# Kernel tuning notes

Measured on AMD Instinct MI355X. Metric: run time of the kernel, lower is better.

The kernel has to match this reference:

```python
import jax, jax.numpy as jnp
import numpy as np

C = 1.0            # PoincareBall curvature
BALL_EPS = 4e-3    # geoopt projx eps for float32
MIN_NORM = 1e-15


def artanh(x):
    x = jnp.clip(x, -1.0 + 1e-7, 1.0 - 1e-7)
    return 0.5 * (jnp.log1p(x) - jnp.log1p(-x))


def project(x):
    # geoopt projx: clip norm to (1 - eps) / sqrt(c)
    norm = jnp.maximum(jnp.linalg.norm(x, axis=-1, keepdims=True), MIN_NORM)
    maxnorm = (1.0 - BALL_EPS) / jnp.sqrt(C)
    return jnp.where(norm > maxnorm, x / norm * maxnorm, x)


def mobius_matvec(M, x):
    # geoopt mobius_matvec on PoincareBall (followed by project)
    sqrt_c = jnp.sqrt(C)
    x_norm = jnp.maximum(jnp.linalg.norm(x, axis=-1, keepdims=True), MIN_NORM)
    mx = x @ M.T
    mx_norm = jnp.maximum(jnp.linalg.norm(mx, axis=-1, keepdims=True), MIN_NORM)
    res = jnp.tanh(mx_norm / x_norm * artanh(sqrt_c * x_norm)) * mx / (mx_norm * sqrt_c)
    zero_mx = jnp.all(mx == 0.0, axis=-1, keepdims=True)
    return project(jnp.where(zero_mx, 0.0, res))


def mobius_add(x, y):
    # geoopt mobius_add on PoincareBall (followed by project)
    x2 = jnp.sum(x * x, axis=-1, keepdims=True)
    y2 = jnp.sum(y * y, axis=-1, keepdims=True)
    xy = jnp.sum(x * y, axis=-1, keepdims=True)
    num = (1.0 + 2.0 * C * xy + C * y2) * x + (1.0 - C * x2) * y
    den = jnp.maximum(1.0 + 2.0 * C * xy + C * C * x2 * y2, MIN_NORM)
    return project(num / den)


def hyp_linear(x, W, b):
    out = mobius_matvec(W, x)
    return mobius_add(out, b)


def hyperbolic_scores(q, k):
    # q, k: [B, H, S, Dh]
    eps = 1e-5
    q_norm_sq = jnp.minimum(jnp.sum(q * q, axis=-1, keepdims=True), 1.0 - eps)  # [B,H,S,1]
    k_norm_sq = jnp.minimum(jnp.sum(k * k, axis=-1, keepdims=True), 1.0 - eps)  # [B,H,S,1]
    qk = jnp.einsum('bhqd,bhkd->bhqk', q, k)
    k_norm_sq_t = jnp.swapaxes(k_norm_sq, -2, -1)                               # [B,H,1,S]
    denom = (1.0 - q_norm_sq) * (1.0 - k_norm_sq_t) + eps
    delta = 2.0 * ((qk - q_norm_sq * k_norm_sq_t) / denom)
    dist_sq = jnp.sqrt(jnp.maximum(delta, eps))
    return -dist_sq


def setup_inputs() -> dict:
    key = jax.random.key(0)
    B, S, E = 4, 2048, 512
    ks = jax.random.split(key, 5)
    x = jax.random.normal(ks[0], (B, S, E), dtype=jnp.float32) * 0.02  # inside unit ball
    bound = float(np.sqrt(6.0 / (E + E)))  # xavier_uniform
    def w(k):
        return jax.random.uniform(k, (E, E), dtype=jnp.float32, minval=-bound, maxval=bound)
    z = jnp.zeros((E,), dtype=jnp.float32)
    return {
        'x': x,
        'Wq': w(ks[1]), 'bq': z,
        'Wk': w(ks[2]), 'bk': z,
        'Wv': w(ks[3]), 'bv': z,
        'Wo': w(ks[4]), 'bo': z,
    }


def reference(x, Wq, bq, Wk, bk, Wv, bv, Wo, bo):
    B, S, E = x.shape
    H = 8
    Dh = E // H
    q = hyp_linear(x, Wq, bq)
    k = hyp_linear(x, Wk, bk)
    v = hyp_linear(x, Wv, bv)
    # [B,S,E] -> [B,H,S,Dh]
    split = lambda t: t.reshape(B, S, H, Dh).transpose(0, 2, 1, 3)
    q, k, v = split(q), split(k), split(v)
    scores = hyperbolic_scores(q, k) / jnp.sqrt(jnp.float32(Dh))
    attn = jax.nn.softmax(scores, axis=-1)
    out = jnp.einsum('bhqk,bhkd->bhqd', attn, v)
    out = out.transpose(0, 2, 1, 3).reshape(B, S, E)
    return hyp_linear(out, Wo, bo)
```

## Files before the change

kernel.cpp:

```cpp
#include <hip/hip_runtime.h>
#include <math.h>

#define B_ 4
#define S_ 2048
#define E_ 512
#define H_ 8
#define Dh_ 64
#define BS_ (B_*S_)
#define MAXN 0.996f

typedef __attribute__((ext_vector_type(8))) short short8;
typedef __attribute__((ext_vector_type(4))) float f32x4;

__device__ __forceinline__ unsigned f2bf(float x) {
  unsigned u = __float_as_uint(x);
  return (u + 0x7fffu + ((u >> 16) & 1u)) >> 16;
}
__device__ __forceinline__ float bf2f(unsigned b) {
  return __uint_as_float(b << 16);
}

__device__ __forceinline__ void gload_lds16(const void* g, void* lds) {
  __builtin_amdgcn_global_load_lds(
      (const __attribute__((address_space(1))) unsigned int*)g,
      (__attribute__((address_space(3))) unsigned int*)lds, 16, 0, 0);
}

__global__ __launch_bounds__(256) void pack_w_kernel(const float* __restrict__ W0,
    const float* __restrict__ W1, const float* __restrict__ W2,
    const float* __restrict__ W3, unsigned short* __restrict__ Wp) {
  const float* W = (blockIdx.y == 0) ? W0 : (blockIdx.y == 1) ? W1
                 : (blockIdx.y == 2) ? W2 : W3;
  unsigned short* dst = Wp + (size_t)blockIdx.y * 262144;
  int l = threadIdx.x & 63, tq = threadIdx.x >> 6;
  int n = blockIdx.x;
  int col = 16*n + (l & 15);
  int k0 = 8 * (l >> 4);
  #pragma unroll
  for (int tt = 0; tt < 4; ++tt) {
    int t = tq*4 + tt;
    const float* wp_ = W + (size_t)col * E_ + 32*t + k0;
    float4 a0 = *(const float4*)wp_, a1 = *(const float4*)(wp_ + 4);
    float av[8] = {a0.x,a0.y,a0.z,a0.w,a1.x,a1.y,a1.z,a1.w};
    short8 hi;
    #pragma unroll
    for (int j = 0; j < 8; ++j) hi[j] = (short)f2bf(av[j]);
    *(short8*)(dst + ((size_t)(t*32 + n))*512 + l*8) = hi;
  }
}

__global__ __launch_bounds__(256, 4) void qkv_linear(const float* __restrict__ X,
    const unsigned short* __restrict__ Wp,
    const float* __restrict__ bq_, const float* __restrict__ bk_,
    const float* __restrict__ bv_,
    unsigned short* __restrict__ Qhi, unsigned short* __restrict__ Khi,
    unsigned short* __restrict__ Vhi,
    float* __restrict__ qn, float* __restrict__ kn) {
  __shared__ float smM[4][4][4], smB[4][4][4], smb2[4];
  int tid = threadIdx.x;
  int w = tid >> 6, l = tid & 63;
  int l15 = l & 15, g = l >> 4;
  int R = blockIdx.x;
  int mat = blockIdx.y;
  const unsigned short* Wm = Wp + (size_t)mat * 262144;
  const float* bvec = (mat == 0) ? bq_ : (mat == 1) ? bk_ : bv_;
  unsigned short* outHi = (mat == 0) ? Qhi : (mat == 1) ? Khi : Vhi;
  float* normOut = (mat == 0) ? qn : kn;

  f32x4 acc[8];
  #pragma unroll
  for (int s = 0; s < 8; ++s) acc[s] = (f32x4){0.f,0.f,0.f,0.f};
  const float* xrow = X + (size_t)(R*16 + l15)*E_ + 8*g;

  float4 c0 = *(const float4*)xrow;
  float4 c1 = *(const float4*)(xrow + 4);
  float xsq = 0.f;

  #pragma unroll 2
  for (int t = 0; t < 16; ++t) {
    float av[8] = {c0.x,c0.y,c0.z,c0.w,c1.x,c1.y,c1.z,c1.w};
    short8 ahi, alo;
    #pragma unroll
    for (int j = 0; j < 8; ++j) {
      unsigned hb = f2bf(av[j]);
      ahi[j] = (short)hb;
      alo[j] = (short)f2bf(av[j] - bf2f(hb));
      xsq = fmaf(av[j], av[j], xsq);
    }
    if (t < 15) {
      c0 = *(const float4*)(xrow + 32*(t+1));
      c1 = *(const float4*)(xrow + 32*(t+1) + 4);
    }
    const unsigned short* wb = Wm + ((size_t)(t*32 + 8*w))*512 + (size_t)l*8;
    #pragma unroll
    for (int s = 0; s < 8; ++s) {
      short8 bhi = *(const short8*)(wb + s*512);
      acc[s] = __builtin_amdgcn_mfma_f32_16x16x32_bf16(ahi, bhi, acc[s], 0, 0, 0);
      acc[s] = __builtin_amdgcn_mfma_f32_16x16x32_bf16(alo, bhi, acc[s], 0, 0, 0);
    }
  }

  xsq += __shfl_xor(xsq, 16, 64);
  xsq += __shfl_xor(xsq, 32, 64);
  float xnv4[4], art4[4];
  #pragma unroll
  for (int i = 0; i < 4; ++i) {
    float s2 = __shfl(xsq, 4*g + i, 64);
    float xnv = fmaxf(sqrtf(s2), 1e-15f);
    float aa = fminf(xnv, 1.f - 1e-7f);
    xnv4[i] = xnv;
    art4[i] = 0.5f * (log1pf(aa) - log1pf(-aa));
  }

  float bl[8];
  #pragma unroll
  for (int s = 0; s < 8; ++s) bl[s] = bvec[16*(8*w+s) + l15];
  float m2p[4] = {0.f,0.f,0.f,0.f}, mbp[4] = {0.f,0.f,0.f,0.f}, b2p = 0.f;
  #pragma unroll
  for (int s = 0; s < 8; ++s) {
    b2p += bl[s]*bl[s];
    #pragma unroll
    for (int i = 0; i < 4; ++i) {
      m2p[i] = fmaf(acc[s][i], acc[s][i], m2p[i]);
      mbp[i] = fmaf(acc[s][i], bl[s], mbp[i]);
    }
  }
  #pragma unroll
  for (int off = 1; off <= 8; off <<= 1) {
    b2p += __shfl_xor(b2p, off, 64);
    #pragma unroll
    for (int i = 0; i < 4; ++i) {
      m2p[i] += __shfl_xor(m2p[i], off, 64);
      mbp[i] += __shfl_xor(mbp[i], off, 64);
    }
  }
  if (l == 0) smb2[w] = b2p;
  if (l15 == 0) {
    #pragma unroll
    for (int i = 0; i < 4; ++i) { smM[w][g][i] = m2p[i]; smB[w][g][i] = mbp[i]; }
  }
  __syncthreads();
  float b2 = smb2[0] + smb2[1] + smb2[2] + smb2[3];
  float G[4], Hc[4];
  #pragma unroll
  for (int i = 0; i < 4; ++i) {
    float m2 = smM[0][g][i]+smM[1][g][i]+smM[2][g][i]+smM[3][g][i];
    float mb = smB[0][g][i]+smB[1][g][i]+smB[2][g][i]+smB[3][g][i];
    float xn = xnv4[i], art = art4[i];
    float mn = fmaxf(sqrtf(m2), 1e-15f);
    float t = tanhf(mn / xn * art);
    float alpha, rn;
    if (m2 > 0.f) { alpha = t / mn; rn = t; } else { alpha = 0.f; rn = 0.f; }
    if (rn > MAXN) { alpha *= MAXN / rn; rn = MAXN; }
    float x2r = rn * rn;
    float xy = alpha * mb;
    float A  = 1.f + 2.f*xy + b2;
    float Bc = 1.f - x2r;
    float den = fmaxf(1.f + 2.f*xy + x2r*b2, 1e-15f);
    float n2v = (A*A*x2r + 2.f*A*Bc*xy + Bc*Bc*b2) / (den*den);
    float nn = fmaxf(sqrtf(n2v), 1e-15f);
    float sc = (nn > MAXN) ? (MAXN / nn) : 1.f;
    G[i]  = sc * A * alpha / den;
    Hc[i] = sc * Bc / den;
  }

  #pragma unroll
  for (int i = 0; i < 4; ++i) {
    int grow = R*16 + 4*g + i;
    int bb = grow >> 11, seq = grow & 2047;
    int tile = seq >> 6;
    float hn0 = 0.f, hn1 = 0.f;
    #pragma unroll
    for (int s = 0; s < 8; ++s) {
      int col = 16*(8*w+s) + l15;
      float v = G[i]*acc[s][i] + Hc[i]*bl[s];
      int h = col >> 6, c = col & 63;
      size_t base;
      if (mat == 2) {
        int kt = (seq >> 5) & 1, gp = (seq >> 3) & 3, jv = seq & 7;
        int dn = c >> 4, lt = (c & 15) | (gp << 4);
        base = ((size_t)((bb*8 + h)*32 + tile))*4096 + (size_t)((kt*4+dn)*64 + lt)*8 + jv;
      } else {
        int nf = (seq >> 4) & 3, lt15 = seq & 15;
        int dt = c >> 5, m = (c >> 3) & 3, j = c & 7;
        base = ((size_t)((bb*8 + h)*32 + tile))*4096 + (size_t)((dt*4+nf)*64 + (lt15|(m<<4)))*8 + j;
      }
      outHi[base] = (unsigned short)f2bf(v);
      if (mat < 2) { if (s < 4) hn0 += v*v; else hn1 += v*v; }
    }
    if (mat < 2) {
      hn0 += __shfl_xor(hn0,1,64); hn0 += __shfl_xor(hn0,2,64);
      hn0 += __shfl_xor(hn0,4,64); hn0 += __shfl_xor(hn0,8,64);
      hn1 += __shfl_xor(hn1,1,64); hn1 += __shfl_xor(hn1,2,64);
      hn1 += __shfl_xor(hn1,4,64); hn1 += __shfl_xor(hn1,8,64);
      if (l15 == 0) {
        normOut[((size_t)(bb*8 + 2*w + 0))*S_ + seq] = fminf(hn0, 1.f - 1e-5f);
        normOut[((size_t)(bb*8 + 2*w + 1))*S_ + seq] = fminf(hn1, 1.f - 1e-5f);
      }
    }
  }
}

__global__ __launch_bounds__(256, 4) void o_linear(const float* __restrict__ X,
    const unsigned short* __restrict__ Wp, const float* __restrict__ bvec,
    float* __restrict__ outF) {
  __shared__ float smM[4][4][4], smB[4][4][4], smb2[4];
  int tid = threadIdx.x;
  int w = tid >> 6, l = tid & 63;
  int l15 = l & 15, g = l >> 4;
  int R = blockIdx.x;

  f32x4 acc[8];
  #pragma unroll
  for (int s = 0; s < 8; ++s) acc[s] = (f32x4){0.f,0.f,0.f,0.f};
  const float* xrow = X + (size_t)(R*16 + l15)*E_ + 8*g;

  float4 c0 = *(const float4*)xrow;
  float4 c1 = *(const float4*)(xrow + 4);
  float xsq = 0.f;

  #pragma unroll 2
  for (int t = 0; t < 16; ++t) {
    float av[8] = {c0.x,c0.y,c0.z,c0.w,c1.x,c1.y,c1.z,c1.w};
    short8 ahi, alo;
    #pragma unroll
    for (int j = 0; j < 8; ++j) {
      unsigned hb = f2bf(av[j]);
      ahi[j] = (short)hb;
      alo[j] = (short)f2bf(av[j] - bf2f(hb));
      xsq = fmaf(av[j], av[j], xsq);
    }
    if (t < 15) {
      c0 = *(const float4*)(xrow + 32*(t+1));
      c1 = *(const float4*)(xrow + 32*(t+1) + 4);
    }
    const unsigned short* wb = Wp + ((size_t)(t*32 + 8*w))*512 + (size_t)l*8;
    #pragma unroll
    for (int s = 0; s < 8; ++s) {
      short8 bhi = *(const short8*)(wb + s*512);
      acc[s] = __builtin_amdgcn_mfma_f32_16x16x32_bf16(ahi, bhi, acc[s], 0, 0, 0);
      acc[s] = __builtin_amdgcn_mfma_f32_16x16x32_bf16(alo, bhi, acc[s], 0, 0, 0);
    }
  }

  xsq += __shfl_xor(xsq, 16, 64);
  xsq += __shfl_xor(xsq, 32, 64);
  float xnv4[4], art4[4];
  #pragma unroll
  for (int i = 0; i < 4; ++i) {
    float s2 = __shfl(xsq, 4*g + i, 64);
    float xnv = fmaxf(sqrtf(s2), 1e-15f);
    float aa = fminf(xnv, 1.f - 1e-7f);
    xnv4[i] = xnv;
    art4[i] = 0.5f * (log1pf(aa) - log1pf(-aa));
  }

  float bl[8];
  #pragma unroll
  for (int s = 0; s < 8; ++s) bl[s] = bvec[16*(8*w+s) + l15];
  float m2p[4] = {0.f,0.f,0.f,0.f}, mbp[4] = {0.f,0.f,0.f,0.f}, b2p = 0.f;
  #pragma unroll
  for (int s = 0; s < 8; ++s) {
    b2p += bl[s]*bl[s];
    #pragma unroll
    for (int i = 0; i < 4; ++i) {
      m2p[i] = fmaf(acc[s][i], acc[s][i], m2p[i]);
      mbp[i] = fmaf(acc[s][i], bl[s], mbp[i]);
    }
  }
  #pragma unroll
  for (int off = 1; off <= 8; off <<= 1) {
    b2p += __shfl_xor(b2p, off, 64);
    #pragma unroll
    for (int i = 0; i < 4; ++i) {
      m2p[i] += __shfl_xor(m2p[i], off, 64);
      mbp[i] += __shfl_xor(mbp[i], off, 64);
    }
  }
  if (l == 0) smb2[w] = b2p;
  if (l15 == 0) {
    #pragma unroll
    for (int i = 0; i < 4; ++i) { smM[w][g][i] = m2p[i]; smB[w][g][i] = mbp[i]; }
  }
  __syncthreads();
  float b2 = smb2[0] + smb2[1] + smb2[2] + smb2[3];
  #pragma unroll
  for (int i = 0; i < 4; ++i) {
    float m2 = smM[0][g][i]+smM[1][g][i]+smM[2][g][i]+smM[3][g][i];
    float mb = smB[0][g][i]+smB[1][g][i]+smB[2][g][i]+smB[3][g][i];
    float xn = xnv4[i], art = art4[i];
    float mn = fmaxf(sqrtf(m2), 1e-15f);
    float t = tanhf(mn / xn * art);
    float alpha, rn;
    if (m2 > 0.f) { alpha = t / mn; rn = t; } else { alpha = 0.f; rn = 0.f; }
    if (rn > MAXN) { alpha *= MAXN / rn; rn = MAXN; }
    float x2r = rn * rn;
    float xy = alpha * mb;
    float A  = 1.f + 2.f*xy + b2;
    float Bc = 1.f - x2r;
    float den = fmaxf(1.f + 2.f*xy + x2r*b2, 1e-15f);
    float n2v = (A*A*x2r + 2.f*A*Bc*xy + Bc*Bc*b2) / (den*den);
    float nn = fmaxf(sqrtf(n2v), 1e-15f);
    float sc = (nn > MAXN) ? (MAXN / nn) : 1.f;
    float G = sc * A * alpha / den;
    float Hc = sc * Bc / den;
    int grow = R*16 + 4*g + i;
    #pragma unroll
    for (int s = 0; s < 8; ++s)
      outF[(size_t)grow*E_ + 16*(8*w+s) + l15] = G*acc[s][i] + Hc*bl[s];
  }
}

__global__ __launch_bounds__(256, 4) void attn_kernel(
    const unsigned short* __restrict__ Qhi, const unsigned short* __restrict__ Khi,
    const unsigned short* __restrict__ Vhi,
    const float* __restrict__ qn_arr, const float* __restrict__ kn_arr,
    float* __restrict__ Out) {
  __shared__ __align__(16) unsigned short Kf[4096];
  __shared__ __align__(16) unsigned short Vf[2][4096];
  __shared__ __align__(16) unsigned short Pf[4][1024];

  int tid = threadIdx.x;
  int w = tid >> 6, l = tid & 63;
  int l15 = l & 15, g = l >> 4;

  int bid = blockIdx.x;
  int xcd = bid & 7, idx = bid >> 3;
  int bh = xcd * 4 + (idx >> 5);
  int qblk = idx & 31;
  int b = bh >> 3, h = bh & 7;
  int qb = qblk * 64;

  const unsigned short* qbase = Qhi + ((size_t)(bh*32 + qblk))*4096;
  short8 qhi[2];
  #pragma unroll
  for (int dt = 0; dt < 2; ++dt)
    qhi[dt] = *(const short8*)(qbase + (size_t)((dt*4 + w)*64 + l)*8);
  float qnv[4], qd[4], rq[4];
  #pragma unroll
  for (int i = 0; i < 4; ++i) {
    qnv[i] = qn_arr[(size_t)bh*S_ + qb + 16*w + 4*g + i];
    qd[i] = 1.f - qnv[i];
    rq[i] = __builtin_amdgcn_rcpf(qd[i]);
  }

  f32x4 Oacc[4];
  #pragma unroll
  for (int dn = 0; dn < 4; ++dn) Oacc[dn] = (f32x4){0.f,0.f,0.f,0.f};
  float lp[4] = {0.f,0.f,0.f,0.f};

  const unsigned short* Kbh = Khi + ((size_t)bh*32)*4096;
  const unsigned short* Vbh = Vhi + ((size_t)bh*32)*4096;
  const float* knp = kn_arr + (size_t)bh*S_;

  #pragma unroll
  for (int r = 0; r < 2; ++r) {
    gload_lds16(Kbh + r*2048 + w*512 + l*8, &Kf[r*2048 + w*512]);
    gload_lds16(Vbh + r*2048 + w*512 + l*8, &Vf[0][r*2048 + w*512]);
  }
  asm volatile("s_waitcnt vmcnt(0)" ::: "memory");
  __syncthreads();

  #pragma unroll 1
  for (int tile = 0; tile < 32; ++tile) {
    int cur = tile & 1;
    int kb = tile * 64;
    float knc[4];
    #pragma unroll
    for (int n = 0; n < 4; ++n) knc[n] = knp[kb + 16*n + l15];
    #pragma unroll
    for (int n = 0; n < 4; ++n) {
      f32x4 Cn = (f32x4){0.f,0.f,0.f,0.f};
      #pragma unroll
      for (int dt = 0; dt < 2; ++dt) {
        short8 kfr = *(const short8*)&Kf[((dt*4 + n)*64 + l)*8];
        Cn = __builtin_amdgcn_mfma_f32_16x16x32_bf16(qhi[dt], kfr, Cn, 0, 0, 0);
      }
      float kd = 1.f - knc[n];
      float rkn = __builtin_amdgcn_rcpf(kd);
      int cbase = (n >> 1)*64 + 16*((2*n + (l15 >> 3)) & 3) + 4*g;
      int csb = cbase ^ ((cbase >> 3) & 7);
      int j7 = l15 & 7;
      #pragma unroll
      for (int i = 0; i < 4; ++i) {
        float num = fmaf(-qnv[i], knc[n], Cn[i]);
        float d2 = fmaxf(num * (rq[i]*rkn), 5e-6f);
        float sq = d2 * __builtin_amdgcn_rsqf(d2);
        float p = __builtin_amdgcn_exp2f(-0.25503386f * sq);
        unsigned u = __float_as_uint(p);
        lp[i] += __uint_as_float(u & 0xffff0000u);
        Pf[w][((csb ^ i) << 3) + j7] = (unsigned short)(u >> 16);
      }
    }
    __builtin_amdgcn_s_barrier();
    if (tile < 31) {
      const unsigned short* kp = Kbh + ((size_t)(tile+1))*4096;
      const unsigned short* vp = Vbh + ((size_t)(tile+1))*4096;
      #pragma unroll
      for (int r = 0; r < 2; ++r)
        gload_lds16(kp + r*2048 + w*512 + l*8, &Kf[r*2048 + w*512]);
      #pragma unroll
      for (int r = 0; r < 2; ++r)
        gload_lds16(vp + r*2048 + w*512 + l*8, &Vf[cur^1][r*2048 + w*512]);
    }
    __builtin_amdgcn_sched_barrier(0);
    short8 pa0, pa1;
    { int c = l;       int cs = c ^ ((c >> 3) & 7); pa0 = *(const short8*)&Pf[w][cs*8]; }
    { int c = 64 + l;  int cs = c ^ ((c >> 3) & 7); pa1 = *(const short8*)&Pf[w][cs*8]; }
    #pragma unroll
    for (int dn = 0; dn < 4; ++dn) {
      short8 v0 = *(const short8*)&Vf[cur][((0*4 + dn)*64 + l)*8];
      short8 v1 = *(const short8*)&Vf[cur][((1*4 + dn)*64 + l)*8];
      f32x4 o = Oacc[dn];
      o = __builtin_amdgcn_mfma_f32_16x16x32_bf16(pa0, v0, o, 0, 0, 0);
      o = __builtin_amdgcn_mfma_f32_16x16x32_bf16(pa1, v1, o, 0, 0, 0);
      Oacc[dn] = o;
    }
    asm volatile("s_waitcnt vmcnt(2)" ::: "memory");
    __builtin_amdgcn_s_barrier();
  }

  #pragma unroll
  for (int i = 0; i < 4; ++i) {
    lp[i] += __shfl_xor(lp[i], 1, 64);
    lp[i] += __shfl_xor(lp[i], 2, 64);
    lp[i] += __shfl_xor(lp[i], 4, 64);
    lp[i] += __shfl_xor(lp[i], 8, 64);
    lp[i] = 1.f / lp[i];
  }
  #pragma unroll
  for (int i = 0; i < 4; ++i) {
    size_t orow = (size_t)(b*S_ + qb + 16*w + 4*g + i)*E_ + h*Dh_;
    #pragma unroll
    for (int dn = 0; dn < 4; ++dn)
      Out[orow + 16*dn + l15] = Oacc[dn][i] * lp[i];
  }
}

extern "C" void kernel_launch(void* const* d_in, const int* in_sizes, int n_in,
                              void* d_out, int out_size, void* d_ws, size_t ws_size,
                              hipStream_t stream) {
  const float* x  = (const float*)d_in[0];
  const float* Wq = (const float*)d_in[1];
  const float* bq = (const float*)d_in[2];
  const float* Wk = (const float*)d_in[3];
  const float* bk = (const float*)d_in[4];
  const float* Wv = (const float*)d_in[5];
  const float* bv = (const float*)d_in[6];
  const float* Wo = (const float*)d_in[7];
  const float* bo = (const float*)d_in[8];
  float* out = (float*)d_out;

  char* p = (char*)d_ws;
  unsigned short* Wp  = (unsigned short*)p; p += (size_t)2  << 20;
  unsigned short* Qhi = (unsigned short*)p; p += (size_t)8  << 20;
  unsigned short* Khi = (unsigned short*)p; p += (size_t)8  << 20;
  unsigned short* Vhi = (unsigned short*)p; p += (size_t)8  << 20;
  float* ao   = (float*)p; p += (size_t)16 << 20;
  float* qn   = (float*)p; p += (size_t)B_*H_*S_ * 4;
  float* kn   = (float*)p; p += (size_t)B_*H_*S_ * 4;

  pack_w_kernel<<<dim3(32, 4), dim3(256), 0, stream>>>(Wq, Wk, Wv, Wo, Wp);
  qkv_linear<<<dim3(BS_/16, 3), dim3(256), 0, stream>>>(x, Wp, bq, bk, bv, Qhi, Khi, Vhi, qn, kn);
  attn_kernel<<<dim3(1024), dim3(256), 0, stream>>>(Qhi, Khi, Vhi, qn, kn, ao);
  o_linear<<<dim3(BS_/16), dim3(256), 0, stream>>>(ao, Wp + 3*262144, bo, out);
}
```

Before: 167.8 us.

## Process 32 rows per block in linear kernels to reuse weight fragments

The QKV and output linear kernels now compute two 16-row tiles per block, so each weight fragment loaded from global memory feeds twice as many MFMAs. This halves the grid size and the total weight traffic. The loop is no longer unrolled and all weight fragments are loaded up front. Register pressure rises from doubling the accumulators, so launch bounds drop from 4 to 3 blocks per CU, which lowers occupancy and the number of blocks available to hide latency.

```diff
diff --git a/kernel.cpp b/kernel.cpp
--- a/kernel.cpp
+++ b/kernel.cpp
@@ -49,14 +49,14 @@
   }
 }
 
-__global__ __launch_bounds__(256, 4) void qkv_linear(const float* __restrict__ X,
+__global__ __launch_bounds__(256, 3) void qkv_linear(const float* __restrict__ X,
     const unsigned short* __restrict__ Wp,
     const float* __restrict__ bq_, const float* __restrict__ bk_,
     const float* __restrict__ bv_,
     unsigned short* __restrict__ Qhi, unsigned short* __restrict__ Khi,
     unsigned short* __restrict__ Vhi,
     float* __restrict__ qn, float* __restrict__ kn) {
-  __shared__ float smM[4][4][4], smB[4][4][4], smb2[4];
+  __shared__ float smM[2][4][4][4], smB[2][4][4][4], smb2[4];
   int tid = threadIdx.x;
   int w = tid >> 6, l = tid & 63;
   int l15 = l & 15, g = l >> 4;
@@ -67,247 +67,311 @@
   unsigned short* outHi = (mat == 0) ? Qhi : (mat == 1) ? Khi : Vhi;
   float* normOut = (mat == 0) ? qn : kn;
 
-  f32x4 acc[8];
-  #pragma unroll
-  for (int s = 0; s < 8; ++s) acc[s] = (f32x4){0.f,0.f,0.f,0.f};
-  const float* xrow = X + (size_t)(R*16 + l15)*E_ + 8*g;
-
-  float4 c0 = *(const float4*)xrow;
-  float4 c1 = *(const float4*)(xrow + 4);
-  float xsq = 0.f;
-
-  #pragma unroll 2
+  f32x4 acc0[8], acc1[8];
+  #pragma unroll
+  for (int s = 0; s < 8; ++s) {
+    acc0[s] = (f32x4){0.f,0.f,0.f,0.f};
+    acc1[s] = (f32x4){0.f,0.f,0.f,0.f};
+  }
+  const float* xrow0 = X + (size_t)(R*32 + l15)*E_ + 8*g;
+  const float* xrow1 = xrow0 + (size_t)16*E_;
+  const unsigned short* wl = Wm + (size_t)(8*w)*512 + (size_t)l*8;
+
+  float4 p00 = *(const float4*)xrow0, p01 = *(const float4*)(xrow0 + 4);
+  float4 p10 = *(const float4*)xrow1, p11 = *(const float4*)(xrow1 + 4);
+  float xsq0 = 0.f, xsq1 = 0.f;
+
+  #pragma unroll 1
   for (int t = 0; t < 16; ++t) {
-    float av[8] = {c0.x,c0.y,c0.z,c0.w,c1.x,c1.y,c1.z,c1.w};
-    short8 ahi, alo;
+    const unsigned short* wb = wl + (size_t)t*16384;
+    short8 b[8];
+    #pragma unroll
+    for (int s = 0; s < 8; ++s) b[s] = *(const short8*)(wb + s*512);
+    float a0v[8] = {p00.x,p00.y,p00.z,p00.w,p01.x,p01.y,p01.z,p01.w};
+    float a1v[8] = {p10.x,p10.y,p10.z,p10.w,p11.x,p11.y,p11.z,p11.w};
+    short8 ahi0, alo0, ahi1, alo1;
     #pragma unroll
     for (int j = 0; j < 8; ++j) {
-      unsigned hb = f2bf(av[j]);
-      ahi[j] = (short)hb;
-      alo[j] = (short)f2bf(av[j] - bf2f(hb));
-      xsq = fmaf(av[j], av[j], xsq);
+      unsigned hb0 = f2bf(a0v[j]);
+      ahi0[j] = (short)hb0;
+      alo0[j] = (short)f2bf(a0v[j] - bf2f(hb0));
+      xsq0 = fmaf(a0v[j], a0v[j], xsq0);
+      unsigned hb1 = f2bf(a1v[j]);
+      ahi1[j] = (short)hb1;
+      alo1[j] = (short)f2bf(a1v[j] - bf2f(hb1));
+      xsq1 = fmaf(a1v[j], a1v[j], xsq1);
     }
     if (t < 15) {
-      c0 = *(const float4*)(xrow + 32*(t+1));
-      c1 = *(const float4*)(xrow + 32*(t+1) + 4);
-    }
-    const unsigned short* wb = Wm + ((size_t)(t*32 + 8*w))*512 + (size_t)l*8;
+      p00 = *(const float4*)(xrow0 + 32*(t+1));
+      p01 = *(const float4*)(xrow0 + 32*(t+1) + 4);
+      p10 = *(const float4*)(xrow1 + 32*(t+1));
+      p11 = *(const float4*)(xrow1 + 32*(t+1) + 4);
+    }
     #pragma unroll
     for (int s = 0; s < 8; ++s) {
-      short8 bhi = *(const short8*)(wb + s*512);
-      acc[s] = __builtin_amdgcn_mfma_f32_16x16x32_bf16(ahi, bhi, acc[s], 0, 0, 0);
-      acc[s] = __builtin_amdgcn_mfma_f32_16x16x32_bf16(alo, bhi, acc[s], 0, 0, 0);
-    }
-  }
-
-  xsq += __shfl_xor(xsq, 16, 64);
-  xsq += __shfl_xor(xsq, 32, 64);
-  float xnv4[4], art4[4];
+      acc0[s] = __builtin_amdgcn_mfma_f32_16x16x32_bf16(ahi0, b[s], acc0[s], 0, 0, 0);
+      acc0[s] = __builtin_amdgcn_mfma_f32_16x16x32_bf16(alo0, b[s], acc0[s], 0, 0, 0);
+      acc1[s] = __builtin_amdgcn_mfma_f32_16x16x32_bf16(ahi1, b[s], acc1[s], 0, 0, 0);
+      acc1[s] = __builtin_amdgcn_mfma_f32_16x16x32_bf16(alo1, b[s], acc1[s], 0, 0, 0);
+    }
+  }
+
+  xsq0 += __shfl_xor(xsq0, 16, 64); xsq0 += __shfl_xor(xsq0, 32, 64);
+  xsq1 += __shfl_xor(xsq1, 16, 64); xsq1 += __shfl_xor(xsq1, 32, 64);
+  float xnv4[2][4], art4[2][4];
   #pragma unroll
   for (int i = 0; i < 4; ++i) {
-    float s2 = __shfl(xsq, 4*g + i, 64);
-    float xnv = fmaxf(sqrtf(s2), 1e-15f);
-    float aa = fminf(xnv, 1.f - 1e-7f);
-    xnv4[i] = xnv;
-    art4[i] = 0.5f * (log1pf(aa) - log1pf(-aa));
+    float s20 = __shfl(xsq0, 4*g + i, 64);
+    float s21 = __shfl(xsq1, 4*g + i, 64);
+    float xn0 = fmaxf(sqrtf(s20), 1e-15f);
+    float xn1 = fmaxf(sqrtf(s21), 1e-15f);
+    float aa0 = fminf(xn0, 1.f - 1e-7f);
+    float aa1 = fminf(xn1, 1.f - 1e-7f);
+    xnv4[0][i] = xn0; art4[0][i] = 0.5f * (log1pf(aa0) - log1pf(-aa0));
+    xnv4[1][i] = xn1; art4[1][i] = 0.5f * (log1pf(aa1) - log1pf(-aa1));
   }
 
   float bl[8];
   #pragma unroll
   for (int s = 0; s < 8; ++s) bl[s] = bvec[16*(8*w+s) + l15];
-  float m2p[4] = {0.f,0.f,0.f,0.f}, mbp[4] = {0.f,0.f,0.f,0.f}, b2p = 0.f;
+  float m2p[2][4] = {{0.f,0.f,0.f,0.f},{0.f,0.f,0.f,0.f}};
+  float mbp[2][4] = {{0.f,0.f,0.f,0.f},{0.f,0.f,0.f,0.f}};
+  float b2p = 0.f;
   #pragma unroll
   for (int s = 0; s < 8; ++s) {
     b2p += bl[s]*bl[s];
     #pragma unroll
     for (int i = 0; i < 4; ++i) {
-      m2p[i] = fmaf(acc[s][i], acc[s][i], m2p[i]);
-      mbp[i] = fmaf(acc[s][i], bl[s], mbp[i]);
+      m2p[0][i] = fmaf(acc0[s][i], acc0[s][i], m2p[0][i]);
+      mbp[0][i] = fmaf(acc0[s][i], bl[s], mbp[0][i]);
+      m2p[1][i] = fmaf(acc1[s][i], acc1[s][i], m2p[1][i]);
+      mbp[1][i] = fmaf(acc1[s][i], bl[s], mbp[1][i]);
     }
   }
   #pragma unroll
   for (int off = 1; off <= 8; off <<= 1) {
     b2p += __shfl_xor(b2p, off, 64);
     #pragma unroll
-    for (int i = 0; i < 4; ++i) {
-      m2p[i] += __shfl_xor(m2p[i], off, 64);
-      mbp[i] += __shfl_xor(mbp[i], off, 64);
-    }
+    for (int rg = 0; rg < 2; ++rg)
+      #pragma unroll
+      for (int i = 0; i < 4; ++i) {
+        m2p[rg][i] += __shfl_xor(m2p[rg][i], off, 64);
+        mbp[rg][i] += __shfl_xor(mbp[rg][i], off, 64);
+      }
   }
   if (l == 0) smb2[w] = b2p;
   if (l15 == 0) {
     #pragma unroll
-    for (int i = 0; i < 4; ++i) { smM[w][g][i] = m2p[i]; smB[w][g][i] = mbp[i]; }
+    for (int rg = 0; rg < 2; ++rg)
+      #pragma unroll
+      for (int i = 0; i < 4; ++i) { smM[rg][w][g][i] = m2p[rg][i]; smB[rg][w][g][i] = mbp[rg][i]; }
   }
   __syncthreads();
   float b2 = smb2[0] + smb2[1] + smb2[2] + smb2[3];
-  float G[4], Hc[4];
-  #pragma unroll
-  for (int i = 0; i < 4; ++i) {
-    float m2 = smM[0][g][i]+smM[1][g][i]+smM[2][g][i]+smM[3][g][i];
-    float mb = smB[0][g][i]+smB[1][g][i]+smB[2][g][i]+smB[3][g][i];
-    float xn = xnv4[i], art = art4[i];
-    float mn = fmaxf(sqrtf(m2), 1e-15f);
-    float t = tanhf(mn / xn * art);
-    float alpha, rn;
-    if (m2 > 0.f) { alpha = t / mn; rn = t; } else { alpha = 0.f; rn = 0.f; }
-    if (rn > MAXN) { alpha *= MAXN / rn; rn = MAXN; }
-    float x2r = rn * rn;
-    float xy = alpha * mb;
-    float A  = 1.f + 2.f*xy + b2;
-    float Bc = 1.f - x2r;
-    float den = fmaxf(1.f + 2.f*xy + x2r*b2, 1e-15f);
-    float n2v = (A*A*x2r + 2.f*A*Bc*xy + Bc*Bc*b2) / (den*den);
-    float nn = fmaxf(sqrtf(n2v), 1e-15f);
-    float sc = (nn > MAXN) ? (MAXN / nn) : 1.f;
-    G[i]  = sc * A * alpha / den;
-    Hc[i] = sc * Bc / den;
-  }
-
-  #pragma unroll
-  for (int i = 0; i < 4; ++i) {
-    int grow = R*16 + 4*g + i;
-    int bb = grow >> 11, seq = grow & 2047;
-    int tile = seq >> 6;
-    float hn0 = 0.f, hn1 = 0.f;
-    #pragma unroll
-    for (int s = 0; s < 8; ++s) {
-      int col = 16*(8*w+s) + l15;
-      float v = G[i]*acc[s][i] + Hc[i]*bl[s];
-      int h = col >> 6, c = col & 63;
-      size_t base;
-      if (mat == 2) {
-        int kt = (seq >> 5) & 1, gp = (seq >> 3) & 3, jv = seq & 7;
-        int dn = c >> 4, lt = (c & 15) | (gp << 4);
-        base = ((size_t)((bb*8 + h)*32 + tile))*4096 + (size_t)((kt*4+dn)*64 + lt)*8 + jv;
-      } else {
-        int nf = (seq >> 4) & 3, lt15 = seq & 15;
-        int dt = c >> 5, m = (c >> 3) & 3, j = c & 7;
-        base = ((size_t)((bb*8 + h)*32 + tile))*4096 + (size_t)((dt*4+nf)*64 + (lt15|(m<<4)))*8 + j;
+  float G[2][4], Hc[2][4];
+  #pragma unroll
+  for (int rg = 0; rg < 2; ++rg)
+    #pragma unroll
+    for (int i = 0; i < 4; ++i) {
+      float m2 = smM[rg][0][g][i]+smM[rg][1][g][i]+smM[rg][2][g][i]+smM[rg][3][g][i];
+      float mb = smB[rg][0][g][i]+smB[rg][1][g][i]+smB[rg][2][g][i]+smB[rg][3][g][i];
+      float xn = xnv4[rg][i], art = art4[rg][i];
+      float mn = fmaxf(sqrtf(m2), 1e-15f);
+      float t = tanhf(mn / xn * art);
+      float alpha, rn;
+      if (m2 > 0.f) { alpha = t / mn; rn = t; } else { alpha = 0.f; rn = 0.f; }
+      if (rn > MAXN) { alpha *= MAXN / rn; rn = MAXN; }
+      float x2r = rn * rn;
+      float xy = alpha * mb;
+      float A  = 1.f + 2.f*xy + b2;
+      float Bc = 1.f - x2r;
+      float den = fmaxf(1.f + 2.f*xy + x2r*b2, 1e-15f);
+      float n2v = (A*A*x2r + 2.f*A*Bc*xy + Bc*Bc*b2) / (den*den);
+      float nn = fmaxf(sqrtf(n2v), 1e-15f);
+      float sc = (nn > MAXN) ? (MAXN / nn) : 1.f;
+      G[rg][i]  = sc * A * alpha / den;
+      Hc[rg][i] = sc * Bc / den;
+    }
+
+  #pragma unroll
+  for (int rg = 0; rg < 2; ++rg) {
+    const f32x4* acc = rg ? acc1 : acc0;
+    #pragma unroll
+    for (int i = 0; i < 4; ++i) {
+      int grow = R*32 + rg*16 + 4*g + i;
+      int bb = grow >> 11, seq = grow & 2047;
+      int tile = seq >> 6;
+      float hn0 = 0.f, hn1 = 0.f;
+      #pragma unroll
+      for (int s = 0; s < 8; ++s) {
+        int col = 16*(8*w+s) + l15;
+        float v = G[rg][i]*acc[s][i] + Hc[rg][i]*bl[s];
+        int h = col >> 6, c = col & 63;
+        size_t base;
+        if (mat == 2) {
+          int kt = (seq >> 5) & 1, gp = (seq >> 3) & 3, jv = seq & 7;
+          int dn = c >> 4, lt = (c & 15) | (gp << 4);
+          base = ((size_t)((bb*8 + h)*32 + tile))*4096 + (size_t)((kt*4+dn)*64 + lt)*8 + jv;
+        } else {
+          int nf = (seq >> 4) & 3, lt15 = seq & 15;
+          int dt = c >> 5, m = (c >> 3) & 3, j = c & 7;
+          base = ((size_t)((bb*8 + h)*32 + tile))*4096 + (size_t)((dt*4+nf)*64 + (lt15|(m<<4)))*8 + j;
+        }
+        outHi[base] = (unsigned short)f2bf(v);
+        if (mat < 2) { if (s < 4) hn0 += v*v; else hn1 += v*v; }
       }
-      outHi[base] = (unsigned short)f2bf(v);
-      if (mat < 2) { if (s < 4) hn0 += v*v; else hn1 += v*v; }
-    }
-    if (mat < 2) {
-      hn0 += __shfl_xor(hn0,1,64); hn0 += __shfl_xor(hn0,2,64);
-      hn0 += __shfl_xor(hn0,4,64); hn0 += __shfl_xor(hn0,8,64);
-      hn1 += __shfl_xor(hn1,1,64); hn1 += __shfl_xor(hn1,2,64);
-      hn1 += __shfl_xor(hn1,4,64); hn1 += __shfl_xor(hn1,8,64);
-      if (l15 == 0) {
-        normOut[((size_t)(bb*8 + 2*w + 0))*S_ + seq] = fminf(hn0, 1.f - 1e-5f);
-        normOut[((size_t)(bb*8 + 2*w + 1))*S_ + seq] = fminf(hn1, 1.f - 1e-5f);
+      if (mat < 2) {
+        hn0 += __shfl_xor(hn0,1,64); hn0 += __shfl_xor(hn0,2,64);
+        hn0 += __shfl_xor(hn0,4,64); hn0 += __shfl_xor(hn0,8,64);
+        hn1 += __shfl_xor(hn1,1,64); hn1 += __shfl_xor(hn1,2,64);
+        hn1 += __shfl_xor(hn1,4,64); hn1 += __shfl_xor(hn1,8,64);
+        if (l15 == 0) {
+          normOut[((size_t)(bb*8 + 2*w + 0))*S_ + seq] = fminf(hn0, 1.f - 1e-5f);
+          normOut[((size_t)(bb*8 + 2*w + 1))*S_ + seq] = fminf(hn1, 1.f - 1e-5f);
+        }
       }
     }
   }
 }
 
-__global__ __launch_bounds__(256, 4) void o_linear(const float* __restrict__ X,
+__global__ __launch_bounds__(256, 3) void o_linear(const float* __restrict__ X,
     const unsigned short* __restrict__ Wp, const float* __restrict__ bvec,
     float* __restrict__ outF) {
-  __shared__ float smM[4][4][4], smB[4][4][4], smb2[4];
+  __shared__ float smM[2][4][4][4], smB[2][4][4][4], smb2[4];
   int tid = threadIdx.x;
   int w = tid >> 6, l = tid & 63;
   int l15 = l & 15, g = l >> 4;
   int R = blockIdx.x;
 
-  f32x4 acc[8];
-  #pragma unroll
-  for (int s = 0; s < 8; ++s) acc[s] = (f32x4){0.f,0.f,0.f,0.f};
-  const float* xrow = X + (size_t)(R*16 + l15)*E_ + 8*g;
-
-  float4 c0 = *(const float4*)xrow;
-  float4 c1 = *(const float4*)(xrow + 4);
-  float xsq = 0.f;
-
-  #pragma unroll 2
+  f32x4 acc0[8], acc1[8];
+  #pragma unroll
+  for (int s = 0; s < 8; ++s) {
+    acc0[s] = (f32x4){0.f,0.f,0.f,0.f};
+    acc1[s] = (f32x4){0.f,0.f,0.f,0.f};
+  }
+  const float* xrow0 = X + (size_t)(R*32 + l15)*E_ + 8*g;
+  const float* xrow1 = xrow0 + (size_t)16*E_;
+  const unsigned short* wl = Wp + (size_t)(8*w)*512 + (size_t)l*8;
+
+  float4 p00 = *(const float4*)xrow0, p01 = *(const float4*)(xrow0 + 4);
+  float4 p10 = *(const float4*)xrow1, p11 = *(const float4*)(xrow1 + 4);
+  float xsq0 = 0.f, xsq1 = 0.f;
+
+  #pragma unroll 1
   for (int t = 0; t < 16; ++t) {
-    float av[8] = {c0.x,c0.y,c0.z,c0.w,c1.x,c1.y,c1.z,c1.w};
-    short8 ahi, alo;
+    const unsigned short* wb = wl + (size_t)t*16384;
+    short8 b[8];
+    #pragma unroll
+    for (int s = 0; s < 8; ++s) b[s] = *(const short8*)(wb + s*512);
+    float a0v[8] = {p00.x,p00.y,p00.z,p00.w,p01.x,p01.y,p01.z,p01.w};
+    float a1v[8] = {p10.x,p10.y,p10.z,p10.w,p11.x,p11.y,p11.z,p11.w};
+    short8 ahi0, alo0, ahi1, alo1;
     #pragma unroll
     for (int j = 0; j < 8; ++j) {
-      unsigned hb = f2bf(av[j]);
-      ahi[j] = (short)hb;
-      alo[j] = (short)f2bf(av[j] - bf2f(hb));
-      xsq = fmaf(av[j], av[j], xsq);
+      unsigned hb0 = f2bf(a0v[j]);
+      ahi0[j] = (short)hb0;
+      alo0[j] = (short)f2bf(a0v[j] - bf2f(hb0));
+      xsq0 = fmaf(a0v[j], a0v[j], xsq0);
+      unsigned hb1 = f2bf(a1v[j]);
+      ahi1[j] = (short)hb1;
+      alo1[j] = (short)f2bf(a1v[j] - bf2f(hb1));
+      xsq1 = fmaf(a1v[j], a1v[j], xsq1);
     }
     if (t < 15) {
-      c0 = *(const float4*)(xrow + 32*(t+1));
-      c1 = *(const float4*)(xrow + 32*(t+1) + 4);
-    }
-    const unsigned short* wb = Wp + ((size_t)(t*32 + 8*w))*512 + (size_t)l*8;
+      p00 = *(const float4*)(xrow0 + 32*(t+1));
+      p01 = *(const float4*)(xrow0 + 32*(t+1) + 4);
+      p10 = *(const float4*)(xrow1 + 32*(t+1));
+      p11 = *(const float4*)(xrow1 + 32*(t+1) + 4);
+    }
     #pragma unroll
     for (int s = 0; s < 8; ++s) {
-      short8 bhi = *(const short8*)(wb + s*512);
-      acc[s] = __builtin_amdgcn_mfma_f32_16x16x32_bf16(ahi, bhi, acc[s], 0, 0, 0);
-      acc[s] = __builtin_amdgcn_mfma_f32_16x16x32_bf16(alo, bhi, acc[s], 0, 0, 0);
-    }
-  }
-
-  xsq += __shfl_xor(xsq, 16, 64);
-  xsq += __shfl_xor(xsq, 32, 64);
-  float xnv4[4], art4[4];
+      acc0[s] = __builtin_amdgcn_mfma_f32_16x16x32_bf16(ahi0, b[s], acc0[s], 0, 0, 0);
+      acc0[s] = __builtin_amdgcn_mfma_f32_16x16x32_bf16(alo0, b[s], acc0[s], 0, 0, 0);
+      acc1[s] = __builtin_amdgcn_mfma_f32_16x16x32_bf16(ahi1, b[s], acc1[s], 0, 0, 0);
+      acc1[s] = __builtin_amdgcn_mfma_f32_16x16x32_bf16(alo1, b[s], acc1[s], 0, 0, 0);
+    }
+  }
+
+  xsq0 += __shfl_xor(xsq0, 16, 64); xsq0 += __shfl_xor(xsq0, 32, 64);
+  xsq1 += __shfl_xor(xsq1, 16, 64); xsq1 += __shfl_xor(xsq1, 32, 64);
+  float xnv4[2][4], art4[2][4];
   #pragma unroll
   for (int i = 0; i < 4; ++i) {
-    float s2 = __shfl(xsq, 4*g + i, 64);
-    float xnv = fmaxf(sqrtf(s2), 1e-15f);
-    float aa = fminf(xnv, 1.f - 1e-7f);
-    xnv4[i] = xnv;
-    art4[i] = 0.5f * (log1pf(aa) - log1pf(-aa));
+    float s20 = __shfl(xsq0, 4*g + i, 64);
+    float s21 = __shfl(xsq1, 4*g + i, 64);
+    float xn0 = fmaxf(sqrtf(s20), 1e-15f);
+    float xn1 = fmaxf(sqrtf(s21), 1e-15f);
+    float aa0 = fminf(xn0, 1.f - 1e-7f);
+    float aa1 = fminf(xn1, 1.f - 1e-7f);
+    xnv4[0][i] = xn0; art4[0][i] = 0.5f * (log1pf(aa0) - log1pf(-aa0));
+    xnv4[1][i] = xn1; art4[1][i] = 0.5f * (log1pf(aa1) - log1pf(-aa1));
   }
 
   float bl[8];
   #pragma unroll
   for (int s = 0; s < 8; ++s) bl[s] = bvec[16*(8*w+s) + l15];
-  float m2p[4] = {0.f,0.f,0.f,0.f}, mbp[4] = {0.f,0.f,0.f,0.f}, b2p = 0.f;
+  float m2p[2][4] = {{0.f,0.f,0.f,0.f},{0.f,0.f,0.f,0.f}};
+  float mbp[2][4] = {{0.f,0.f,0.f,0.f},{0.f,0.f,0.f,0.f}};
+  float b2p = 0.f;
   #pragma unroll
   for (int s = 0; s < 8; ++s) {
     b2p += bl[s]*bl[s];
     #pragma unroll
     for (int i = 0; i < 4; ++i) {
-      m2p[i] = fmaf(acc[s][i], acc[s][i], m2p[i]);
-      mbp[i] = fmaf(acc[s][i], bl[s], mbp[i]);
+      m2p[0][i] = fmaf(acc0[s][i], acc0[s][i], m2p[0][i]);
+      mbp[0][i] = fmaf(acc0[s][i], bl[s], mbp[0][i]);
+      m2p[1][i] = fmaf(acc1[s][i], acc1[s][i], m2p[1][i]);
+      mbp[1][i] = fmaf(acc1[s][i], bl[s], mbp[1][i]);
     }
   }
   #pragma unroll
   for (int off = 1; off <= 8; off <<= 1) {
     b2p += __shfl_xor(b2p, off, 64);
     #pragma unroll
-    for (int i = 0; i < 4; ++i) {
-      m2p[i] += __shfl_xor(m2p[i], off, 64);
-      mbp[i] += __shfl_xor(mbp[i], off, 64);
-    }
+    for (int rg = 0; rg < 2; ++rg)
+      #pragma unroll
+      for (int i = 0; i < 4; ++i) {
+        m2p[rg][i] += __shfl_xor(m2p[rg][i], off, 64);
+        mbp[rg][i] += __shfl_xor(mbp[rg][i], off, 64);
+      }
   }
   if (l == 0) smb2[w] = b2p;
   if (l15 == 0) {
     #pragma unroll
-    for (int i = 0; i < 4; ++i) { smM[w][g][i] = m2p[i]; smB[w][g][i] = mbp[i]; }
+    for (int rg = 0; rg < 2; ++rg)
+      #pragma unroll
+      for (int i = 0; i < 4; ++i) { smM[rg][w][g][i] = m2p[rg][i]; smB[rg][w][g][i] = mbp[rg][i]; }
   }
   __syncthreads();
   float b2 = smb2[0] + smb2[1] + smb2[2] + smb2[3];
   #pragma unroll
-  for (int i = 0; i < 4; ++i) {
-    float m2 = smM[0][g][i]+smM[1][g][i]+smM[2][g][i]+smM[3][g][i];
-    float mb = smB[0][g][i]+smB[1][g][i]+smB[2][g][i]+smB[3][g][i];
-    float xn = xnv4[i], art = art4[i];
-    float mn = fmaxf(sqrtf(m2), 1e-15f);
-    float t = tanhf(mn / xn * art);
-    float alpha, rn;
-    if (m2 > 0.f) { alpha = t / mn; rn = t; } else { alpha = 0.f; rn = 0.f; }
-    if (rn > MAXN) { alpha *= MAXN / rn; rn = MAXN; }
-    float x2r = rn * rn;
-    float xy = alpha * mb;
-    float A  = 1.f + 2.f*xy + b2;
-    float Bc = 1.f - x2r;
-    float den = fmaxf(1.f + 2.f*xy + x2r*b2, 1e-15f);
-    float n2v = (A*A*x2r + 2.f*A*Bc*xy + Bc*Bc*b2) / (den*den);
-    float nn = fmaxf(sqrtf(n2v), 1e-15f);
-    float sc = (nn > MAXN) ? (MAXN / nn) : 1.f;
-    float G = sc * A * alpha / den;
-    float Hc = sc * Bc / den;
-    int grow = R*16 + 4*g + i;
-    #pragma unroll
-    for (int s = 0; s < 8; ++s)
-      outF[(size_t)grow*E_ + 16*(8*w+s) + l15] = G*acc[s][i] + Hc*bl[s];
+  for (int rg = 0; rg < 2; ++rg) {
+    const f32x4* acc = rg ? acc1 : acc0;
+    #pragma unroll
+    for (int i = 0; i < 4; ++i) {
+      float m2 = smM[rg][0][g][i]+smM[rg][1][g][i]+smM[rg][2][g][i]+smM[rg][3][g][i];
+      float mb = smB[rg][0][g][i]+smB[rg][1][g][i]+smB[rg][2][g][i]+smB[rg][3][g][i];
+      float xn = xnv4[rg][i], art = art4[rg][i];
+      float mn = fmaxf(sqrtf(m2), 1e-15f);
+      float t = tanhf(mn / xn * art);
+      float alpha, rn;
+      if (m2 > 0.f) { alpha = t / mn; rn = t; } else { alpha = 0.f; rn = 0.f; }
+      if (rn > MAXN) { alpha *= MAXN / rn; rn = MAXN; }
+      float x2r = rn * rn;
+      float xy = alpha * mb;
+      float A  = 1.f + 2.f*xy + b2;
+      float Bc = 1.f - x2r;
+      float den = fmaxf(1.f + 2.f*xy + x2r*b2, 1e-15f);
+      float n2v = (A*A*x2r + 2.f*A*Bc*xy + Bc*Bc*b2) / (den*den);
+      float nn = fmaxf(sqrtf(n2v), 1e-15f);
+      float sc = (nn > MAXN) ? (MAXN / nn) : 1.f;
+      float Gv = sc * A * alpha / den;
+      float Hv = sc * Bc / den;
+      int grow = R*32 + rg*16 + 4*g + i;
+      #pragma unroll
+      for (int s = 0; s < 8; ++s)
+        outF[(size_t)grow*E_ + 16*(8*w+s) + l15] = Gv*acc[s][i] + Hv*bl[s];
+    }
   }
 }
 
@@ -461,7 +525,7 @@
   float* kn   = (float*)p; p += (size_t)B_*H_*S_ * 4;
 
   pack_w_kernel<<<dim3(32, 4), dim3(256), 0, stream>>>(Wq, Wk, Wv, Wo, Wp);
-  qkv_linear<<<dim3(BS_/16, 3), dim3(256), 0, stream>>>(x, Wp, bq, bk, bv, Qhi, Khi, Vhi, qn, kn);
+  qkv_linear<<<dim3(BS_/32, 3), dim3(256), 0, stream>>>(x, Wp, bq, bk, bv, Qhi, Khi, Vhi, qn, kn);
   attn_kernel<<<dim3(1024), dim3(256), 0, stream>>>(Qhi, Khi, Vhi, qn, kn, ao);
-  o_linear<<<dim3(BS_/16), dim3(256), 0, stream>>>(ao, Wp + 3*262144, bo, out);
-}
+  o_linear<<<dim3(BS_/32), dim3(256), 0, stream>>>(ao, Wp + 3*262144, bo, out);
+}
```

New measurement: 160.5 us. 1.05x faster.
